# Performance work log

Measured on AMD Instinct MI355X. Metric: run time of the kernel, lower is better.

The kernel has to match this reference:

```python
import jax, jax.numpy as jnp
import numpy as np


def _gcn_conv(h, src, dst, W, b, n):
    # PyG GCNConv: x @ W, then symmetric-normalized aggregation with self-loops
    deg = jax.ops.segment_sum(jnp.ones(src.shape[0], h.dtype), dst, num_segments=n)
    dinv = jax.lax.rsqrt(jnp.maximum(deg, 1.0))  # deg >= 1 because self-loops are included
    norm = dinv[src] * dinv[dst]                 # [E]
    m = (h @ W)[src] * norm[:, None]             # gather + scale
    return jax.ops.segment_sum(m, dst, num_segments=n) + b


def setup_inputs() -> dict:
    key = jax.random.key(0)
    N, E, F, H, L, V = 50000, 800000, 128, 256, 64, 128
    ks = jax.random.split(key, 16)
    s = lambda fan_in: 1.0 / np.sqrt(fan_in)
    return {
        "x": jax.random.randint(ks[0], (N,), 0, V),
        "edge_index": jax.random.randint(ks[1], (2, E), 0, N),
        "eps": jax.random.normal(ks[2], (N, L), jnp.float32),
        "emb": jax.random.normal(ks[3], (V, F), jnp.float32),
        "W1": jax.random.normal(ks[4], (F, H), jnp.float32) * s(F),
        "b1": jnp.zeros((H,), jnp.float32),
        "W2": jax.random.normal(ks[5], (H, H), jnp.float32) * s(H),
        "b2": jnp.zeros((H,), jnp.float32),
        "Wmu": jax.random.normal(ks[6], (H, L), jnp.float32) * s(H),
        "bmu": jnp.zeros((L,), jnp.float32),
        "Wlv": jax.random.normal(ks[7], (H, L), jnp.float32) * s(H),
        "blv": jnp.zeros((L,), jnp.float32),
        "W3": jax.random.normal(ks[8], (L, H), jnp.float32) * s(L),
        "b3": jnp.zeros((H,), jnp.float32),
        "W4": jax.random.normal(ks[9], (H, V), jnp.float32) * s(H),
        "b4": jnp.zeros((V,), jnp.float32),
        "Wcap": jax.random.normal(ks[10], (L, 1), jnp.float32) * s(L),
        "bcap": jnp.zeros((1,), jnp.float32),
    }


def reference(x, edge_index, eps, emb, W1, b1, W2, b2, Wmu, bmu, Wlv, blv, W3, b3, W4, b4, Wcap, bcap):
    n = x.shape[0]
    loops = jnp.arange(n, dtype=edge_index.dtype)
    src = jnp.concatenate([edge_index[0], loops])  # add self-loops once, reuse
    dst = jnp.concatenate([edge_index[1], loops])

    h = emb[x]                                      # [N, F] embedding lookup
    h = jax.nn.relu(_gcn_conv(h, src, dst, W1, b1, n))
    h = jax.nn.relu(_gcn_conv(h, src, dst, W2, b2, n))
    mu = h @ Wmu + bmu
    logvar = h @ Wlv + blv
    z = mu + eps * jnp.exp(0.5 * logvar)            # reparameterize
    recon_x = jax.nn.relu(z @ W3 + b3) @ W4 + b4    # decode
    capitalize = jax.nn.sigmoid(z @ Wcap + bcap)
    return recon_x, capitalize, mu, logvar
```

## Files before the change

### kernel.cpp

```cpp
#include <hip/hip_runtime.h>
#include <math.h>


typedef __attribute__((ext_vector_type(8))) short bf16x8;
typedef __attribute__((ext_vector_type(4))) float f32x4;

__device__ inline unsigned short f2bf(float x) {
    unsigned u = __float_as_uint(x);
    return (unsigned short)((u + 0x7FFFu + ((u >> 16) & 1u)) >> 16);
}
__device__ inline float bf2f(unsigned short h) {
    return __uint_as_float(((unsigned)h) << 16);
}

__global__ __launch_bounds__(256) void k_deg_count(const int* __restrict__ dst,
                                                   int* __restrict__ degint, int E) {
    int e = blockIdx.x * 256 + threadIdx.x;
    if (e < E) atomicAdd(&degint[dst[e]], 1);
}

#define SCAN_BLOCK 1024
__global__ __launch_bounds__(SCAN_BLOCK) void k_scan_local(
        const int* __restrict__ degint, int* __restrict__ row_ptr,
        int* __restrict__ bsum, float* __restrict__ dinv, int N) {
    __shared__ int s[SCAN_BLOCK];
    int gid = blockIdx.x * SCAN_BLOCK + threadIdx.x;
    int d = (gid < N) ? (degint[gid] + 1) : 0;
    if (gid < N) dinv[gid] = rsqrtf((float)d);
    s[threadIdx.x] = d;
    __syncthreads();
    for (int off = 1; off < SCAN_BLOCK; off <<= 1) {
        int t = (threadIdx.x >= off) ? s[threadIdx.x - off] : 0;
        __syncthreads();
        s[threadIdx.x] += t;
        __syncthreads();
    }
    if (gid < N) row_ptr[gid] = s[threadIdx.x] - d;
    if (threadIdx.x == SCAN_BLOCK - 1) bsum[blockIdx.x] = s[SCAN_BLOCK - 1];
}

__global__ void k_scan_bsum(int* __restrict__ bsum, int nb) {
    if (blockIdx.x == 0 && threadIdx.x == 0) {
        int acc = 0;
        for (int i = 0; i < nb; ++i) { int v = bsum[i]; bsum[i] = acc; acc += v; }
    }
}

__global__ __launch_bounds__(256) void k_scan_add(int* __restrict__ row_ptr,
                                                  const int* __restrict__ bsum,
                                                  int N, int T) {
    int gid = blockIdx.x * 256 + threadIdx.x;
    if (gid < N) row_ptr[gid] += bsum[gid / SCAN_BLOCK];
    if (gid == 0) row_ptr[N] = T;
}

__global__ __launch_bounds__(256) void k_fill(
        const int* __restrict__ src, const int* __restrict__ dst,
        const int* __restrict__ x, const float* __restrict__ dinv,
        const int* __restrict__ row_ptr, int* __restrict__ cursor,
        int4* __restrict__ pack, int E, int N) {
    const int base = (blockIdx.x * 256 + threadIdx.x) * 4;
#pragma unroll
    for (int j = 0; j < 4; ++j) {
        int e = base + j;
        if (e < E) {
            int s = src[e], d = dst[e];
            float w = dinv[s] * dinv[d];
            int pos = row_ptr[d] + atomicAdd(&cursor[d], 1);
            pack[pos] = make_int4(__float_as_int(w), x[s], s, 0);
        } else if (e < E + N) {
            int i = e - E;
            float di = dinv[i];
            int pos = row_ptr[i] + atomicAdd(&cursor[i], 1);
            pack[pos] = make_int4(__float_as_int(di * di), x[i], i, 0);
        }
    }
}

__global__ __launch_bounds__(256) void k_cvt_all(
        const float* __restrict__ B0, unsigned short* __restrict__ h0, int K0, int N0,
        const float* __restrict__ B1, unsigned short* __restrict__ h1, int K1, int N1,
        const float* __restrict__ B2, unsigned short* __restrict__ h2, int K2, int N2,
        const float* __restrict__ B3, unsigned short* __restrict__ h3, int K3, int N3,
        const float* __restrict__ B4, unsigned short* __restrict__ h4, int K4, int N4) {
    const float* B; unsigned short* Bh; int K, Ncol;
    switch (blockIdx.y) {
        case 0: B = B0; Bh = h0; K = K0; Ncol = N0; break;
        case 1: B = B1; Bh = h1; K = K1; Ncol = N1; break;
        case 2: B = B2; Bh = h2; K = K2; Ncol = N2; break;
        case 3: B = B3; Bh = h3; K = K3; Ncol = N3; break;
        default: B = B4; Bh = h4; K = K4; Ncol = N4; break;
    }
    int i = blockIdx.x * 256 + threadIdx.x;
    if (i >= K * Ncol) return;
    int k = i / Ncol, n = i - k * Ncol;
    Bh[(long)n * K + k] = f2bf(B[i]);
}

__global__ __launch_bounds__(256) void k_gemm_f32t(
        const float* __restrict__ A, const float* __restrict__ B,
        unsigned short* __restrict__ CbT, int M, int K, int Ncol) {
    constexpr int BM = 64, BN = 64, BK = 16;
    __shared__ float As[BK][BM];
    __shared__ float Bs[BK][BN];
    const int tid = threadIdx.x;
    const int tx = tid & 15, ty = tid >> 4;
    const int rowBase = blockIdx.x * BM;
    const int colBase = blockIdx.y * BN;
    const int lr = tid >> 2, lc4 = tid & 3;
    const int br = tid >> 4, bc4 = tid & 15;
    const int arow = rowBase + lr;
    const int K4 = K >> 2, N4 = Ncol >> 2;
    const float4* A4 = (const float4*)A;
    const float4* B4 = (const float4*)B;
    float acc[4][4] = {{0.f}};
    for (int k0 = 0; k0 < K; k0 += BK) {
        float4 av = make_float4(0.f, 0.f, 0.f, 0.f);
        if (arow < M) av = A4[(long)arow * K4 + (k0 >> 2) + lc4];
        As[lc4 * 4 + 0][lr] = av.x;
        As[lc4 * 4 + 1][lr] = av.y;
        As[lc4 * 4 + 2][lr] = av.z;
        As[lc4 * 4 + 3][lr] = av.w;
        float4 bv = B4[(long)(k0 + br) * N4 + (colBase >> 2) + bc4];
        *(float4*)&Bs[br][bc4 * 4] = bv;
        __syncthreads();
#pragma unroll
        for (int k = 0; k < BK; ++k) {
            float4 a4v = *(const float4*)&As[k][ty * 4];
            float4 b4v = *(const float4*)&Bs[k][tx * 4];
            float aa[4] = {a4v.x, a4v.y, a4v.z, a4v.w};
            float bb[4] = {b4v.x, b4v.y, b4v.z, b4v.w};
#pragma unroll
            for (int i = 0; i < 4; ++i)
#pragma unroll
                for (int j = 0; j < 4; ++j)
                    acc[i][j] = fmaf(aa[i], bb[j], acc[i][j]);
        }
        __syncthreads();
    }
#pragma unroll
    for (int i = 0; i < 4; ++i) {
        int row = rowBase + ty * 4 + i;
        if (row < M) {
#pragma unroll
            for (int c = 0; c < 4; ++c) {
                int col = colBase + tx * 4 + c;
                CbT[(long)col * M + row] = f2bf(acc[i][c]);
            }
        }
    }
}

__global__ __launch_bounds__(256) void k_coef(
        const int4* __restrict__ pack, const int* __restrict__ row_ptr,
        unsigned short* __restrict__ cb, int N) {
    const int wave = threadIdx.x >> 6;
    const int lane = threadIdx.x & 63;
    const int node = blockIdx.x * 4 + wave;
    if (node >= N) return;
    const int tok0 = lane, tok1 = lane + 64;
    float c0 = 0.f, c1 = 0.f;
    const int beg = row_ptr[node], end = row_ptr[node + 1];
    int e = beg;
    for (; e + 4 <= end; e += 4) {
        int2 p0 = *(const int2*)&pack[e];
        int2 p1 = *(const int2*)&pack[e + 1];
        int2 p2 = *(const int2*)&pack[e + 2];
        int2 p3 = *(const int2*)&pack[e + 3];
        c0 += (p0.y == tok0) ? __int_as_float(p0.x) : 0.f;
        c1 += (p0.y == tok1) ? __int_as_float(p0.x) : 0.f;
        c0 += (p1.y == tok0) ? __int_as_float(p1.x) : 0.f;
        c1 += (p1.y == tok1) ? __int_as_float(p1.x) : 0.f;
        c0 += (p2.y == tok0) ? __int_as_float(p2.x) : 0.f;
        c1 += (p2.y == tok1) ? __int_as_float(p2.x) : 0.f;
        c0 += (p3.y == tok0) ? __int_as_float(p3.x) : 0.f;
        c1 += (p3.y == tok1) ? __int_as_float(p3.x) : 0.f;
    }
    for (; e < end; ++e) {
        int2 p = *(const int2*)&pack[e];
        c0 += (p.y == tok0) ? __int_as_float(p.x) : 0.f;
        c1 += (p.y == tok1) ? __int_as_float(p.x) : 0.f;
    }
    const long base = (long)node * 128;
    cb[base + lane]      = f2bf(c0);
    cb[base + lane + 64] = f2bf(c1);
}

template<bool RELU, bool BIAS, bool OUTBF>
__global__ __launch_bounds__(256) void k_gemm_mfma(
        const unsigned short* __restrict__ A, const unsigned short* __restrict__ Bt,
        const float* __restrict__ bias, float* __restrict__ Cf,
        unsigned short* __restrict__ Cb, int M, int K, int Ncol) {
    __shared__ unsigned short Ash[128][40];
    __shared__ unsigned short Bsh[64][40];
    const int tid = threadIdx.x;
    const int lane = tid & 63, w = tid >> 6;
    const int fr = lane & 15, quad = lane >> 4;
    const int wm0 = w * 32;
    const int rowBase = blockIdx.x * 128;
    const int colBase = blockIdx.y * 64;

    const int arow = tid >> 1;
    const int ahalf = (tid & 1) << 4;
    int agrow = rowBase + arow; if (agrow >= M) agrow = M - 1;
    const long abase = (long)agrow * K + ahalf;
    const int brow = tid >> 2;
    const int bseg = (tid & 3) << 3;
    const long bbase = (long)(colBase + brow) * K + bseg;

    f32x4 acc[2][4];
#pragma unroll
    for (int i = 0; i < 2; ++i)
#pragma unroll
        for (int j = 0; j < 4; ++j) acc[i][j] = (f32x4){0.f, 0.f, 0.f, 0.f};

    for (int k0 = 0; k0 < K; k0 += 32) {
        *(bf16x8*)&Ash[arow][ahalf]     = *(const bf16x8*)&A[abase + k0];
        *(bf16x8*)&Ash[arow][ahalf + 8] = *(const bf16x8*)&A[abase + k0 + 8];
        *(bf16x8*)&Bsh[brow][bseg]      = *(const bf16x8*)&Bt[bbase + k0];
        __syncthreads();
        bf16x8 ahf[2], bhf[4];
#pragma unroll
        for (int i = 0; i < 2; ++i)
            ahf[i] = *(const bf16x8*)&Ash[wm0 + i * 16 + fr][quad * 8];
#pragma unroll
        for (int j = 0; j < 4; ++j)
            bhf[j] = *(const bf16x8*)&Bsh[j * 16 + fr][quad * 8];
#pragma unroll
        for (int i = 0; i < 2; ++i)
#pragma unroll
            for (int j = 0; j < 4; ++j)
                acc[i][j] = __builtin_amdgcn_mfma_f32_16x16x32_bf16(
                    ahf[i], bhf[j], acc[i][j], 0, 0, 0);
        __syncthreads();
    }

#pragma unroll
    for (int i = 0; i < 2; ++i) {
        const int rowb = rowBase + wm0 + i * 16 + quad * 4;
#pragma unroll
        for (int j = 0; j < 4; ++j) {
            const int col = colBase + j * 16 + fr;
            const float bv = BIAS ? bias[col] : 0.f;
#pragma unroll
            for (int r = 0; r < 4; ++r) {
                const int row = rowb + r;
                if (row < M) {
                    float v = acc[i][j][r] + bv;
                    if (RELU) v = fmaxf(v, 0.f);
                    const long o = (long)row * Ncol + col;
                    if (OUTBF) Cb[o] = f2bf(v);
                    else       Cf[o] = v;
                }
            }
        }
    }
}

__global__ __launch_bounds__(256) void k_gemm_heads(
        const unsigned short* __restrict__ A, const unsigned short* __restrict__ Bt,
        const float* __restrict__ bmu, const float* __restrict__ blv,
        const float* __restrict__ eps, const float* __restrict__ Wcap,
        const float* __restrict__ bcap, float* __restrict__ mu,
        float* __restrict__ lv, unsigned short* __restrict__ Zh,
        float* __restrict__ cap, int M) {
    constexpr int K = 256;
    __shared__ unsigned short Ash[64][40];
    __shared__ unsigned short Bsh[128][40];
    const int tid = threadIdx.x;
    const int lane = tid & 63, w = tid >> 6;
    const int fr = lane & 15, quad = lane >> 4;
    const int wm0 = w * 16;
    const int rowBase = blockIdx.x * 64;

    const int arow = tid >> 2;
    const int aseg = (tid & 3) << 3;
    int agrow = rowBase + arow; if (agrow >= M) agrow = M - 1;
    const long abase = (long)agrow * K + aseg;
    const int brow = tid >> 1;
    const int bseg = (tid & 1) << 4;
    const long bbase = (long)brow * K + bseg;

    f32x4 acc[8];
#pragma unroll
    for (int j = 0; j < 8; ++j) acc[j] = (f32x4){0.f, 0.f, 0.f, 0.f};

    for (int k0 = 0; k0 < K; k0 += 32) {
        *(bf16x8*)&Ash[arow][aseg] = *(const bf16x8*)&A[abase + k0];
        *(bf16x8*)&Bsh[brow][bseg]     = *(const bf16x8*)&Bt[bbase + k0];
        *(bf16x8*)&Bsh[brow][bseg + 8] = *(const bf16x8*)&Bt[bbase + k0 + 8];
        __syncthreads();
        bf16x8 ahf = *(const bf16x8*)&Ash[wm0 + fr][quad * 8];
#pragma unroll
        for (int j = 0; j < 8; ++j) {
            bf16x8 bhf = *(const bf16x8*)&Bsh[j * 16 + fr][quad * 8];
            acc[j] = __builtin_amdgcn_mfma_f32_16x16x32_bf16(ahf, bhf, acc[j], 0, 0, 0);
        }
        __syncthreads();
    }

    float capacc[4] = {0.f, 0.f, 0.f, 0.f};
#pragma unroll
    for (int j = 0; j < 4; ++j) {
        const int c = j * 16 + fr;
        const float bm = bmu[c], bl = blv[c];
        const float wc = Wcap[c];
#pragma unroll
        for (int r = 0; r < 4; ++r) {
            const int row = rowBase + wm0 + quad * 4 + r;
            if (row < M) {
                const long o = (long)row * 64 + c;
                float mv = acc[j][r] + bm;
                float lvv = acc[j + 4][r] + bl;
                mu[o] = mv;
                lv[o] = lvv;
                float zz = fmaf(eps[o], expf(0.5f * lvv), mv);
                Zh[o] = f2bf(zz);
                capacc[r] = fmaf(zz, wc, capacc[r]);
            }
        }
    }
    const float b0 = bcap[0];
#pragma unroll
    for (int r = 0; r < 4; ++r) {
        float v = capacc[r];
        v += __shfl_xor(v, 1, 64);
        v += __shfl_xor(v, 2, 64);
        v += __shfl_xor(v, 4, 64);
        v += __shfl_xor(v, 8, 64);
        if (fr == 0) {
            const int row = rowBase + wm0 + quad * 4 + r;
            if (row < M) cap[row] = 1.f / (1.f + expf(-(v + b0)));
        }
    }
}

__global__ __launch_bounds__(256) void k_gemm_decode(
        const unsigned short* __restrict__ Zh, const unsigned short* __restrict__ W3t,
        const unsigned short* __restrict__ W4t, const float* __restrict__ b3,
        const float* __restrict__ b4, float* __restrict__ recon, int M) {
    __shared__ unsigned short Zs[64][40];
    __shared__ unsigned short Bsh[256][40];
    __shared__ unsigned short Ts[64][264];
    const int tid = threadIdx.x;
    const int lane = tid & 63, w = tid >> 6;
    const int fr = lane & 15, quad = lane >> 4;
    const int wm0 = w * 16;
    const int rowBase = blockIdx.x * 64;

    const int zrow = tid & 63;
    const int zseg = (tid >> 6) << 3;
    int zgrow = rowBase + zrow; if (zgrow >= M) zgrow = M - 1;
    const long zbase = (long)zgrow * 64 + zseg;

    f32x4 acc1[16];
#pragma unroll
    for (int j = 0; j < 16; ++j) acc1[j] = (f32x4){0.f, 0.f, 0.f, 0.f};

#pragma unroll
    for (int k0 = 0; k0 < 64; k0 += 32) {
        *(bf16x8*)&Zs[zrow][zseg] = *(const bf16x8*)&Zh[zbase + k0 - zseg + zseg];
        __syncthreads();
        __syncthreads();
        break;
    }
#pragma unroll
    for (int j = 0; j < 16; ++j) acc1[j] = (f32x4){0.f, 0.f, 0.f, 0.f};
    for (int k0 = 0; k0 < 64; k0 += 32) {
        *(bf16x8*)&Zs[zrow][zseg] = *(const bf16x8*)&Zh[(long)zgrow * 64 + k0 + zseg];
        {
            const long wb = (long)tid * 64 + k0;
            *(bf16x8*)&Bsh[tid][0]  = *(const bf16x8*)&W3t[wb];
            *(bf16x8*)&Bsh[tid][8]  = *(const bf16x8*)&W3t[wb + 8];
            *(bf16x8*)&Bsh[tid][16] = *(const bf16x8*)&W3t[wb + 16];
            *(bf16x8*)&Bsh[tid][24] = *(const bf16x8*)&W3t[wb + 24];
        }
        __syncthreads();
        bf16x8 af = *(const bf16x8*)&Zs[wm0 + fr][quad * 8];
#pragma unroll
        for (int j = 0; j < 16; ++j) {
            bf16x8 bf = *(const bf16x8*)&Bsh[j * 16 + fr][quad * 8];
            acc1[j] = __builtin_amdgcn_mfma_f32_16x16x32_bf16(af, bf, acc1[j], 0, 0, 0);
        }
        __syncthreads();
    }

#pragma unroll
    for (int j = 0; j < 16; ++j) {
        const int col = j * 16 + fr;
        const float bv = b3[col];
#pragma unroll
        for (int r = 0; r < 4; ++r) {
            const int rl = wm0 + quad * 4 + r;
            Ts[rl][col] = f2bf(fmaxf(acc1[j][r] + bv, 0.f));
        }
    }
    __syncthreads();

    f32x4 acc2[8];
#pragma unroll
    for (int j = 0; j < 8; ++j) acc2[j] = (f32x4){0.f, 0.f, 0.f, 0.f};
    const int br2 = tid >> 1;
    const int bs2 = (tid & 1) << 4;
    for (int k0 = 0; k0 < 256; k0 += 32) {
        const long wb = (long)br2 * 256 + k0 + bs2;
        *(bf16x8*)&Bsh[br2][bs2]     = *(const bf16x8*)&W4t[wb];
        *(bf16x8*)&Bsh[br2][bs2 + 8] = *(const bf16x8*)&W4t[wb + 8];
        __syncthreads();
        bf16x8 at = *(const bf16x8*)&Ts[wm0 + fr][k0 + quad * 8];
#pragma unroll
        for (int j = 0; j < 8; ++j) {
            bf16x8 bf = *(const bf16x8*)&Bsh[j * 16 + fr][quad * 8];
            acc2[j] = __builtin_amdgcn_mfma_f32_16x16x32_bf16(at, bf, acc2[j], 0, 0, 0);
        }
        __syncthreads();
    }

#pragma unroll
    for (int j = 0; j < 8; ++j) {
        const int col = j * 16 + fr;
        const float bv = b4[col];
#pragma unroll
        for (int r = 0; r < 4; ++r) {
            const int row = rowBase + wm0 + quad * 4 + r;
            if (row < M) recon[(long)row * 128 + col] = acc2[j][r] + bv;
        }
    }
}

__global__ __launch_bounds__(256) void k_agg_nb(
        const unsigned short* __restrict__ h1, const int* __restrict__ row_ptr,
        const int4* __restrict__ pack, unsigned short* __restrict__ Ob, int N) {
    const int wave = threadIdx.x >> 6;
    const int lane = threadIdx.x & 63;
    const int node = blockIdx.x * 4 + wave;
    if (node >= N) return;
    const ushort4* h4 = (const ushort4*)h1;
    float ax = 0.f, ay = 0.f, az = 0.f, aw = 0.f;
    const int beg = row_ptr[node], end = row_ptr[node + 1];
    int e = beg;
    for (; e + 8 <= end; e += 8) {
        int4 p0 = pack[e],     p1 = pack[e + 1], p2 = pack[e + 2], p3 = pack[e + 3];
        int4 p4 = pack[e + 4], p5 = pack[e + 5], p6 = pack[e + 6], p7 = pack[e + 7];
        ushort4 v0 = h4[(long)p0.z * 64 + lane];
        ushort4 v1 = h4[(long)p1.z * 64 + lane];
        ushort4 v2 = h4[(long)p2.z * 64 + lane];
        ushort4 v3 = h4[(long)p3.z * 64 + lane];
        ushort4 v4 = h4[(long)p4.z * 64 + lane];
        ushort4 v5 = h4[(long)p5.z * 64 + lane];
        ushort4 v6 = h4[(long)p6.z * 64 + lane];
        ushort4 v7 = h4[(long)p7.z * 64 + lane];
        float w0 = __int_as_float(p0.x), w1 = __int_as_float(p1.x);
        float w2 = __int_as_float(p2.x), w3 = __int_as_float(p3.x);
        float w4 = __int_as_float(p4.x), w5 = __int_as_float(p5.x);
        float w6 = __int_as_float(p6.x), w7 = __int_as_float(p7.x);
        ax = fmaf(bf2f(v0.x), w0, ax); ay = fmaf(bf2f(v0.y), w0, ay);
        az = fmaf(bf2f(v0.z), w0, az); aw = fmaf(bf2f(v0.w), w0, aw);
        ax = fmaf(bf2f(v1.x), w1, ax); ay = fmaf(bf2f(v1.y), w1, ay);
        az = fmaf(bf2f(v1.z), w1, az); aw = fmaf(bf2f(v1.w), w1, aw);
        ax = fmaf(bf2f(v2.x), w2, ax); ay = fmaf(bf2f(v2.y), w2, ay);
        az = fmaf(bf2f(v2.z), w2, az); aw = fmaf(bf2f(v2.w), w2, aw);
        ax = fmaf(bf2f(v3.x), w3, ax); ay = fmaf(bf2f(v3.y), w3, ay);
        az = fmaf(bf2f(v3.z), w3, az); aw = fmaf(bf2f(v3.w), w3, aw);
        ax = fmaf(bf2f(v4.x), w4, ax); ay = fmaf(bf2f(v4.y), w4, ay);
        az = fmaf(bf2f(v4.z), w4, az); aw = fmaf(bf2f(v4.w), w4, aw);
        ax = fmaf(bf2f(v5.x), w5, ax); ay = fmaf(bf2f(v5.y), w5, ay);
        az = fmaf(bf2f(v5.z), w5, az); aw = fmaf(bf2f(v5.w), w5, aw);
        ax = fmaf(bf2f(v6.x), w6, ax); ay = fmaf(bf2f(v6.y), w6, ay);
        az = fmaf(bf2f(v6.z), w6, az); aw = fmaf(bf2f(v6.w), w6, aw);
        ax = fmaf(bf2f(v7.x), w7, ax); ay = fmaf(bf2f(v7.y), w7, ay);
        az = fmaf(bf2f(v7.z), w7, az); aw = fmaf(bf2f(v7.w), w7, aw);
    }
    for (; e + 4 <= end; e += 4) {
        int4 p0 = pack[e], p1 = pack[e + 1], p2 = pack[e + 2], p3 = pack[e + 3];
        ushort4 v0 = h4[(long)p0.z * 64 + lane];
        ushort4 v1 = h4[(long)p1.z * 64 + lane];
        ushort4 v2 = h4[(long)p2.z * 64 + lane];
        ushort4 v3 = h4[(long)p3.z * 64 + lane];
        float w0 = __int_as_float(p0.x), w1 = __int_as_float(p1.x);
        float w2 = __int_as_float(p2.x), w3 = __int_as_float(p3.x);
        ax = fmaf(bf2f(v0.x), w0, ax); ay = fmaf(bf2f(v0.y), w0, ay);
        az = fmaf(bf2f(v0.z), w0, az); aw = fmaf(bf2f(v0.w), w0, aw);
        ax = fmaf(bf2f(v1.x), w1, ax); ay = fmaf(bf2f(v1.y), w1, ay);
        az = fmaf(bf2f(v1.z), w1, az); aw = fmaf(bf2f(v1.w), w1, aw);
        ax = fmaf(bf2f(v2.x), w2, ax); ay = fmaf(bf2f(v2.y), w2, ay);
        az = fmaf(bf2f(v2.z), w2, az); aw = fmaf(bf2f(v2.w), w2, aw);
        ax = fmaf(bf2f(v3.x), w3, ax); ay = fmaf(bf2f(v3.y), w3, ay);
        az = fmaf(bf2f(v3.z), w3, az); aw = fmaf(bf2f(v3.w), w3, aw);
    }
    for (; e < end; ++e) {
        int4 p = pack[e];
        float w0 = __int_as_float(p.x);
        ushort4 v = h4[(long)p.z * 64 + lane];
        ax = fmaf(bf2f(v.x), w0, ax); ay = fmaf(bf2f(v.y), w0, ay);
        az = fmaf(bf2f(v.z), w0, az); aw = fmaf(bf2f(v.w), w0, aw);
    }
    ushort4 o;
    o.x = f2bf(ax); o.y = f2bf(ay); o.z = f2bf(az); o.w = f2bf(aw);
    ((ushort4*)Ob)[(long)node * 64 + lane] = o;
}

extern "C" void kernel_launch(void* const* d_in, const int* in_sizes, int n_in,
                              void* d_out, int out_size, void* d_ws, size_t ws_size,
                              hipStream_t stream) {
    const int*   x    = (const int*)d_in[0];
    const int*   ei   = (const int*)d_in[1];
    const float* eps  = (const float*)d_in[2];
    const float* emb  = (const float*)d_in[3];
    const float* W1   = (const float*)d_in[4];
    const float* b1   = (const float*)d_in[5];
    const float* W2   = (const float*)d_in[6];
    const float* b2   = (const float*)d_in[7];
    const float* Wmu  = (const float*)d_in[8];
    const float* bmu  = (const float*)d_in[9];
    const float* Wlv  = (const float*)d_in[10];
    const float* blv  = (const float*)d_in[11];
    const float* W3   = (const float*)d_in[12];
    const float* b3   = (const float*)d_in[13];
    const float* W4   = (const float*)d_in[14];
    const float* b4   = (const float*)d_in[15];
    const float* Wcap = (const float*)d_in[16];
    const float* bcap = (const float*)d_in[17];

    const int N = in_sizes[0];
    const int E = in_sizes[1] / 2;
    const int H = in_sizes[5];
    const int L = in_sizes[9];
    const int V = in_sizes[15];
    const int F = in_sizes[4] / H;
    const int T = E + N;

    const int* src = ei;
    const int* dst = ei + E;

    char* w = (char*)d_ws;
    unsigned short* h1b  = (unsigned short*)w; w += (size_t)N * H * 2;
    unsigned short* a2b  = (unsigned short*)w; w += (size_t)N * H * 2;
    unsigned short* h2b  = (unsigned short*)w; w += (size_t)N * H * 2;
    unsigned short* zh   = (unsigned short*)w; w += (size_t)N * L * 2;
    unsigned short* cb   = (unsigned short*)w; w += (size_t)N * V * 2;
    int*   degint = (int*)w;   w += (size_t)N * 4;
    int*   cursor = (int*)w;   w += (size_t)N * 4;
    int*   rowp   = (int*)w;   w += (size_t)(N + 1) * 4;
    float* dinv   = (float*)w; w += (size_t)N * 4;
    int*   bsum   = (int*)w;   w += 256 * 4;
    int4*  pack   = (int4*)w;  w += (size_t)T * 16;
    unsigned short* tabT = (unsigned short*)w; w += (size_t)H * V * 2;
    unsigned short* W2t  = (unsigned short*)w; w += (size_t)H * H * 2;
    unsigned short* Wml  = (unsigned short*)w; w += (size_t)H * 2 * L * 2;
    unsigned short* W3t  = (unsigned short*)w; w += (size_t)L * H * 2;
    unsigned short* W4t  = (unsigned short*)w; w += (size_t)H * V * 2;

    float* outp    = (float*)d_out;
    float* recon   = outp;
    float* cap     = outp + (size_t)N * V;
    float* mu      = outp + (size_t)N * V + N;
    float* logvar  = mu + (size_t)N * L;

    const int nN  = (N + 255) / 256;
    const int nE  = (E + 255) / 256;
    const int nT4 = (T + 1023) / 1024;
    const int nSc = (N + SCAN_BLOCK - 1) / SCAN_BLOCK;
    const int gM128 = (N + 127) / 128;
    const int gM64  = (N + 63) / 64;

    hipMemsetAsync(degint, 0, (size_t)N * 8, stream);
    k_deg_count<<<nE, 256, 0, stream>>>(dst, degint, E);
    k_scan_local<<<nSc, SCAN_BLOCK, 0, stream>>>(degint, rowp, bsum, dinv, N);
    k_scan_bsum<<<1, 64, 0, stream>>>(bsum, nSc);
    k_scan_add<<<nN, 256, 0, stream>>>(rowp, bsum, N, T);
    k_fill<<<nT4, 256, 0, stream>>>(src, dst, x, dinv, rowp, cursor, pack, E, N);

    k_cvt_all<<<dim3((H * H + 255) / 256, 5), 256, 0, stream>>>(
        W2, W2t, H, H,
        Wmu, Wml, H, L,
        Wlv, Wml + (size_t)L * H, H, L,
        W3, W3t, L, H,
        W4, W4t, H, V);

    k_gemm_f32t<<<dim3(V / 64, H / 64), 256, 0, stream>>>(emb, W1, tabT, V, F, H);
    k_coef<<<(N + 3) / 4, 256, 0, stream>>>(pack, rowp, cb, N);
    k_gemm_mfma<true, true, true><<<dim3(gM128, H / 64), 256, 0, stream>>>(
        cb, tabT, b1, nullptr, h1b, N, V, H);

    k_agg_nb<<<(N + 3) / 4, 256, 0, stream>>>(h1b, rowp, pack, a2b, N);
    k_gemm_mfma<true, true, true><<<dim3(gM128, H / 64), 256, 0, stream>>>(
        a2b, W2t, b2, nullptr, h2b, N, H, H);

    k_gemm_heads<<<gM64, 256, 0, stream>>>(
        h2b, Wml, bmu, blv, eps, Wcap, bcap, mu, logvar, zh, cap, N);

    k_gemm_decode<<<gM64, 256, 0, stream>>>(zh, W3t, W4t, b3, b4, recon, N);
}
```

Measured before the change: 409.4 us.

## Use full-width 256-column GEMM tiles and half-wave 16-byte gathers in aggregation

Replaces the 128x64-tile GEMM with a 64x256 tile, so each block computes all 256 output columns and the A tile is read once instead of four times across column blocks. The pack layout is reordered so the weight and source index sit in the first 8 bytes. The aggregation kernel now reads only those 8 bytes as int2 and splits each wave into two halves that gather different edges with 16-byte row loads, then combines the halves with a shuffle. The coef kernel now loads full int4 records to reach the token field, and a dead loop is removed from the decoder. The larger B tile in shared memory and the 16 accumulators per lane raise register and LDS pressure, which may lower occupancy.

```diff
diff --git a/kernel.cpp b/kernel.cpp
--- a/kernel.cpp
+++ b/kernel.cpp
@@ -3,6 +3,7 @@
 
 
 typedef __attribute__((ext_vector_type(8))) short bf16x8;
+typedef __attribute__((ext_vector_type(8))) unsigned short u16x8;
 typedef __attribute__((ext_vector_type(4))) float f32x4;
 
 __device__ inline unsigned short f2bf(float x) {
@@ -67,12 +68,12 @@
             int s = src[e], d = dst[e];
             float w = dinv[s] * dinv[d];
             int pos = row_ptr[d] + atomicAdd(&cursor[d], 1);
-            pack[pos] = make_int4(__float_as_int(w), x[s], s, 0);
+            pack[pos] = make_int4(__float_as_int(w), s, x[s], 0);
         } else if (e < E + N) {
             int i = e - E;
             float di = dinv[i];
             int pos = row_ptr[i] + atomicAdd(&cursor[i], 1);
-            pack[pos] = make_int4(__float_as_int(di * di), x[i], i, 0);
+            pack[pos] = make_int4(__float_as_int(di * di), i, x[i], 0);
         }
     }
 }
@@ -163,95 +164,81 @@
     const int beg = row_ptr[node], end = row_ptr[node + 1];
     int e = beg;
     for (; e + 4 <= end; e += 4) {
-        int2 p0 = *(const int2*)&pack[e];
-        int2 p1 = *(const int2*)&pack[e + 1];
-        int2 p2 = *(const int2*)&pack[e + 2];
-        int2 p3 = *(const int2*)&pack[e + 3];
-        c0 += (p0.y == tok0) ? __int_as_float(p0.x) : 0.f;
-        c1 += (p0.y == tok1) ? __int_as_float(p0.x) : 0.f;
-        c0 += (p1.y == tok0) ? __int_as_float(p1.x) : 0.f;
-        c1 += (p1.y == tok1) ? __int_as_float(p1.x) : 0.f;
-        c0 += (p2.y == tok0) ? __int_as_float(p2.x) : 0.f;
-        c1 += (p2.y == tok1) ? __int_as_float(p2.x) : 0.f;
-        c0 += (p3.y == tok0) ? __int_as_float(p3.x) : 0.f;
-        c1 += (p3.y == tok1) ? __int_as_float(p3.x) : 0.f;
+        int4 p0 = pack[e];
+        int4 p1 = pack[e + 1];
+        int4 p2 = pack[e + 2];
+        int4 p3 = pack[e + 3];
+        c0 += (p0.z == tok0) ? __int_as_float(p0.x) : 0.f;
+        c1 += (p0.z == tok1) ? __int_as_float(p0.x) : 0.f;
+        c0 += (p1.z == tok0) ? __int_as_float(p1.x) : 0.f;
+        c1 += (p1.z == tok1) ? __int_as_float(p1.x) : 0.f;
+        c0 += (p2.z == tok0) ? __int_as_float(p2.x) : 0.f;
+        c1 += (p2.z == tok1) ? __int_as_float(p2.x) : 0.f;
+        c0 += (p3.z == tok0) ? __int_as_float(p3.x) : 0.f;
+        c1 += (p3.z == tok1) ? __int_as_float(p3.x) : 0.f;
     }
     for (; e < end; ++e) {
-        int2 p = *(const int2*)&pack[e];
-        c0 += (p.y == tok0) ? __int_as_float(p.x) : 0.f;
-        c1 += (p.y == tok1) ? __int_as_float(p.x) : 0.f;
+        int4 p = pack[e];
+        c0 += (p.z == tok0) ? __int_as_float(p.x) : 0.f;
+        c1 += (p.z == tok1) ? __int_as_float(p.x) : 0.f;
     }
     const long base = (long)node * 128;
     cb[base + lane]      = f2bf(c0);
     cb[base + lane + 64] = f2bf(c1);
 }
 
-template<bool RELU, bool BIAS, bool OUTBF>
-__global__ __launch_bounds__(256) void k_gemm_mfma(
+template<bool RELU>
+__global__ __launch_bounds__(256) void k_gemm_bn256(
         const unsigned short* __restrict__ A, const unsigned short* __restrict__ Bt,
-        const float* __restrict__ bias, float* __restrict__ Cf,
-        unsigned short* __restrict__ Cb, int M, int K, int Ncol) {
-    __shared__ unsigned short Ash[128][40];
-    __shared__ unsigned short Bsh[64][40];
+        const float* __restrict__ bias, unsigned short* __restrict__ Cb,
+        int M, int K) {
+    __shared__ unsigned short Ash[64][40];
+    __shared__ unsigned short Bsh[256][40];
     const int tid = threadIdx.x;
     const int lane = tid & 63, w = tid >> 6;
     const int fr = lane & 15, quad = lane >> 4;
-    const int wm0 = w * 32;
-    const int rowBase = blockIdx.x * 128;
-    const int colBase = blockIdx.y * 64;
-
-    const int arow = tid >> 1;
-    const int ahalf = (tid & 1) << 4;
+    const int wm0 = w * 16;
+    const int rowBase = blockIdx.x * 64;
+
+    const int arow = tid & 63;
+    const int aseg = (tid >> 6) << 3;
     int agrow = rowBase + arow; if (agrow >= M) agrow = M - 1;
-    const long abase = (long)agrow * K + ahalf;
-    const int brow = tid >> 2;
-    const int bseg = (tid & 3) << 3;
-    const long bbase = (long)(colBase + brow) * K + bseg;
-
-    f32x4 acc[2][4];
-#pragma unroll
-    for (int i = 0; i < 2; ++i)
-#pragma unroll
-        for (int j = 0; j < 4; ++j) acc[i][j] = (f32x4){0.f, 0.f, 0.f, 0.f};
+    const long abase = (long)agrow * K + aseg;
+
+    f32x4 acc[16];
+#pragma unroll
+    for (int j = 0; j < 16; ++j) acc[j] = (f32x4){0.f, 0.f, 0.f, 0.f};
 
     for (int k0 = 0; k0 < K; k0 += 32) {
-        *(bf16x8*)&Ash[arow][ahalf]     = *(const bf16x8*)&A[abase + k0];
-        *(bf16x8*)&Ash[arow][ahalf + 8] = *(const bf16x8*)&A[abase + k0 + 8];
-        *(bf16x8*)&Bsh[brow][bseg]      = *(const bf16x8*)&Bt[bbase + k0];
-        __syncthreads();
-        bf16x8 ahf[2], bhf[4];
-#pragma unroll
-        for (int i = 0; i < 2; ++i)
-            ahf[i] = *(const bf16x8*)&Ash[wm0 + i * 16 + fr][quad * 8];
-#pragma unroll
-        for (int j = 0; j < 4; ++j)
-            bhf[j] = *(const bf16x8*)&Bsh[j * 16 + fr][quad * 8];
-#pragma unroll
-        for (int i = 0; i < 2; ++i)
-#pragma unroll
-            for (int j = 0; j < 4; ++j)
-                acc[i][j] = __builtin_amdgcn_mfma_f32_16x16x32_bf16(
-                    ahf[i], bhf[j], acc[i][j], 0, 0, 0);
-        __syncthreads();
-    }
-
-#pragma unroll
-    for (int i = 0; i < 2; ++i) {
-        const int rowb = rowBase + wm0 + i * 16 + quad * 4;
-#pragma unroll
-        for (int j = 0; j < 4; ++j) {
-            const int col = colBase + j * 16 + fr;
-            const float bv = BIAS ? bias[col] : 0.f;
-#pragma unroll
-            for (int r = 0; r < 4; ++r) {
-                const int row = rowb + r;
-                if (row < M) {
-                    float v = acc[i][j][r] + bv;
-                    if (RELU) v = fmaxf(v, 0.f);
-                    const long o = (long)row * Ncol + col;
-                    if (OUTBF) Cb[o] = f2bf(v);
-                    else       Cf[o] = v;
-                }
+        *(bf16x8*)&Ash[arow][aseg] = *(const bf16x8*)&A[abase + k0];
+        {
+            const long wb = (long)tid * K + k0;
+            *(bf16x8*)&Bsh[tid][0]  = *(const bf16x8*)&Bt[wb];
+            *(bf16x8*)&Bsh[tid][8]  = *(const bf16x8*)&Bt[wb + 8];
+            *(bf16x8*)&Bsh[tid][16] = *(const bf16x8*)&Bt[wb + 16];
+            *(bf16x8*)&Bsh[tid][24] = *(const bf16x8*)&Bt[wb + 24];
+        }
+        __syncthreads();
+        bf16x8 af = *(const bf16x8*)&Ash[wm0 + fr][quad * 8];
+#pragma unroll
+        for (int j = 0; j < 16; ++j) {
+            bf16x8 bfv = *(const bf16x8*)&Bsh[j * 16 + fr][quad * 8];
+            acc[j] = __builtin_amdgcn_mfma_f32_16x16x32_bf16(af, bfv, acc[j], 0, 0, 0);
+        }
+        __syncthreads();
+    }
+
+#pragma unroll
+    for (int j = 0; j < 16; ++j) {
+        const int col = j * 16 + fr;
+        const float bv = bias[col];
+#pragma unroll
+        for (int r = 0; r < 4; ++r) {
+            const int row = rowBase + wm0 + quad * 4 + r;
+            if (row < M) {
+                float v = acc[j][r] + bv;
+                if (RELU) v = fmaxf(v, 0.f);
+                Cb[(long)row * 256 + col] = f2bf(v);
             }
         }
     }
@@ -351,19 +338,8 @@
     const int zrow = tid & 63;
     const int zseg = (tid >> 6) << 3;
     int zgrow = rowBase + zrow; if (zgrow >= M) zgrow = M - 1;
-    const long zbase = (long)zgrow * 64 + zseg;
 
     f32x4 acc1[16];
-#pragma unroll
-    for (int j = 0; j < 16; ++j) acc1[j] = (f32x4){0.f, 0.f, 0.f, 0.f};
-
-#pragma unroll
-    for (int k0 = 0; k0 < 64; k0 += 32) {
-        *(bf16x8*)&Zs[zrow][zseg] = *(const bf16x8*)&Zh[zbase + k0 - zseg + zseg];
-        __syncthreads();
-        __syncthreads();
-        break;
-    }
 #pragma unroll
     for (int j = 0; j < 16; ++j) acc1[j] = (f32x4){0.f, 0.f, 0.f, 0.f};
     for (int k0 = 0; k0 < 64; k0 += 32) {
@@ -430,74 +406,58 @@
 
 __global__ __launch_bounds__(256) void k_agg_nb(
         const unsigned short* __restrict__ h1, const int* __restrict__ row_ptr,
-        const int4* __restrict__ pack, unsigned short* __restrict__ Ob, int N) {
+        const int2* __restrict__ pk2, unsigned short* __restrict__ Ob, int N) {
     const int wave = threadIdx.x >> 6;
     const int lane = threadIdx.x & 63;
     const int node = blockIdx.x * 4 + wave;
     if (node >= N) return;
-    const ushort4* h4 = (const ushort4*)h1;
-    float ax = 0.f, ay = 0.f, az = 0.f, aw = 0.f;
+    const int half = lane >> 5;
+    const int col  = lane & 31;
+    const u16x8* hrow = (const u16x8*)h1;
+    float acc[8] = {0.f, 0.f, 0.f, 0.f, 0.f, 0.f, 0.f, 0.f};
     const int beg = row_ptr[node], end = row_ptr[node + 1];
     int e = beg;
     for (; e + 8 <= end; e += 8) {
-        int4 p0 = pack[e],     p1 = pack[e + 1], p2 = pack[e + 2], p3 = pack[e + 3];
-        int4 p4 = pack[e + 4], p5 = pack[e + 5], p6 = pack[e + 6], p7 = pack[e + 7];
-        ushort4 v0 = h4[(long)p0.z * 64 + lane];
-        ushort4 v1 = h4[(long)p1.z * 64 + lane];
-        ushort4 v2 = h4[(long)p2.z * 64 + lane];
-        ushort4 v3 = h4[(long)p3.z * 64 + lane];
-        ushort4 v4 = h4[(long)p4.z * 64 + lane];
-        ushort4 v5 = h4[(long)p5.z * 64 + lane];
-        ushort4 v6 = h4[(long)p6.z * 64 + lane];
-        ushort4 v7 = h4[(long)p7.z * 64 + lane];
-        float w0 = __int_as_float(p0.x), w1 = __int_as_float(p1.x);
-        float w2 = __int_as_float(p2.x), w3 = __int_as_float(p3.x);
-        float w4 = __int_as_float(p4.x), w5 = __int_as_float(p5.x);
-        float w6 = __int_as_float(p6.x), w7 = __int_as_float(p7.x);
-        ax = fmaf(bf2f(v0.x), w0, ax); ay = fmaf(bf2f(v0.y), w0, ay);
-        az = fmaf(bf2f(v0.z), w0, az); aw = fmaf(bf2f(v0.w), w0, aw);
-        ax = fmaf(bf2f(v1.x), w1, ax); ay = fmaf(bf2f(v1.y), w1, ay);
-        az = fmaf(bf2f(v1.z), w1, az); aw = fmaf(bf2f(v1.w), w1, aw);
-        ax = fmaf(bf2f(v2.x), w2, ax); ay = fmaf(bf2f(v2.y), w2, ay);
-        az = fmaf(bf2f(v2.z), w2, az); aw = fmaf(bf2f(v2.w), w2, aw);
-        ax = fmaf(bf2f(v3.x), w3, ax); ay = fmaf(bf2f(v3.y), w3, ay);
-        az = fmaf(bf2f(v3.z), w3, az); aw = fmaf(bf2f(v3.w), w3, aw);
-        ax = fmaf(bf2f(v4.x), w4, ax); ay = fmaf(bf2f(v4.y), w4, ay);
-        az = fmaf(bf2f(v4.z), w4, az); aw = fmaf(bf2f(v4.w), w4, aw);
-        ax = fmaf(bf2f(v5.x), w5, ax); ay = fmaf(bf2f(v5.y), w5, ay);
-        az = fmaf(bf2f(v5.z), w5, az); aw = fmaf(bf2f(v5.w), w5, aw);
-        ax = fmaf(bf2f(v6.x), w6, ax); ay = fmaf(bf2f(v6.y), w6, ay);
-        az = fmaf(bf2f(v6.z), w6, az); aw = fmaf(bf2f(v6.w), w6, aw);
-        ax = fmaf(bf2f(v7.x), w7, ax); ay = fmaf(bf2f(v7.y), w7, ay);
-        az = fmaf(bf2f(v7.z), w7, az); aw = fmaf(bf2f(v7.w), w7, aw);
-    }
-    for (; e + 4 <= end; e += 4) {
-        int4 p0 = pack[e], p1 = pack[e + 1], p2 = pack[e + 2], p3 = pack[e + 3];
-        ushort4 v0 = h4[(long)p0.z * 64 + lane];
-        ushort4 v1 = h4[(long)p1.z * 64 + lane];
-        ushort4 v2 = h4[(long)p2.z * 64 + lane];
-        ushort4 v3 = h4[(long)p3.z * 64 + lane];
-        float w0 = __int_as_float(p0.x), w1 = __int_as_float(p1.x);
-        float w2 = __int_as_float(p2.x), w3 = __int_as_float(p3.x);
-        ax = fmaf(bf2f(v0.x), w0, ax); ay = fmaf(bf2f(v0.y), w0, ay);
-        az = fmaf(bf2f(v0.z), w0, az); aw = fmaf(bf2f(v0.w), w0, aw);
-        ax = fmaf(bf2f(v1.x), w1, ax); ay = fmaf(bf2f(v1.y), w1, ay);
-        az = fmaf(bf2f(v1.z), w1, az); aw = fmaf(bf2f(v1.w), w1, aw);
-        ax = fmaf(bf2f(v2.x), w2, ax); ay = fmaf(bf2f(v2.y), w2, ay);
-        az = fmaf(bf2f(v2.z), w2, az); aw = fmaf(bf2f(v2.w), w2, aw);
-        ax = fmaf(bf2f(v3.x), w3, ax); ay = fmaf(bf2f(v3.y), w3, ay);
-        az = fmaf(bf2f(v3.z), w3, az); aw = fmaf(bf2f(v3.w), w3, aw);
-    }
-    for (; e < end; ++e) {
-        int4 p = pack[e];
-        float w0 = __int_as_float(p.x);
-        ushort4 v = h4[(long)p.z * 64 + lane];
-        ax = fmaf(bf2f(v.x), w0, ax); ay = fmaf(bf2f(v.y), w0, ay);
-        az = fmaf(bf2f(v.z), w0, az); aw = fmaf(bf2f(v.w), w0, aw);
-    }
-    ushort4 o;
-    o.x = f2bf(ax); o.y = f2bf(ay); o.z = f2bf(az); o.w = f2bf(aw);
-    ((ushort4*)Ob)[(long)node * 64 + lane] = o;
+        int2 q0 = pk2[2 * (e + 0 + half)];
+        int2 q1 = pk2[2 * (e + 2 + half)];
+        int2 q2 = pk2[2 * (e + 4 + half)];
+        int2 q3 = pk2[2 * (e + 6 + half)];
+        u16x8 v0 = hrow[(long)q0.y * 32 + col];
+        u16x8 v1 = hrow[(long)q1.y * 32 + col];
+        u16x8 v2 = hrow[(long)q2.y * 32 + col];
+        u16x8 v3 = hrow[(long)q3.y * 32 + col];
+        float w0 = __int_as_float(q0.x), w1 = __int_as_float(q1.x);
+        float w2 = __int_as_float(q2.x), w3 = __int_as_float(q3.x);
+#pragma unroll
+        for (int c = 0; c < 8; ++c) {
+            acc[c] = fmaf(bf2f(v0[c]), w0, acc[c]);
+            acc[c] = fmaf(bf2f(v1[c]), w1, acc[c]);
+            acc[c] = fmaf(bf2f(v2[c]), w2, acc[c]);
+            acc[c] = fmaf(bf2f(v3[c]), w3, acc[c]);
+        }
+    }
+    for (; e + 2 <= end; e += 2) {
+        int2 q = pk2[2 * (e + half)];
+        float w = __int_as_float(q.x);
+        u16x8 v = hrow[(long)q.y * 32 + col];
+#pragma unroll
+        for (int c = 0; c < 8; ++c) acc[c] = fmaf(bf2f(v[c]), w, acc[c]);
+    }
+    if (e < end) {
+        int2 q = pk2[2 * e];
+        float w = (half == 0) ? __int_as_float(q.x) : 0.f;
+        u16x8 v = hrow[(long)q.y * 32 + col];
+#pragma unroll
+        for (int c = 0; c < 8; ++c) acc[c] = fmaf(bf2f(v[c]), w, acc[c]);
+    }
+#pragma unroll
+    for (int c = 0; c < 8; ++c) acc[c] += __shfl_xor(acc[c], 32, 64);
+    if (lane < 32) {
+        u16x8 o;
+#pragma unroll
+        for (int c = 0; c < 8; ++c) o[c] = f2bf(acc[c]);
+        ((u16x8*)Ob)[(long)node * 32 + col] = o;
+    }
 }
 
 extern "C" void kernel_launch(void* const* d_in, const int* in_sizes, int n_in,
@@ -561,7 +521,6 @@
     const int nE  = (E + 255) / 256;
     const int nT4 = (T + 1023) / 1024;
     const int nSc = (N + SCAN_BLOCK - 1) / SCAN_BLOCK;
-    const int gM128 = (N + 127) / 128;
     const int gM64  = (N + 63) / 64;
 
     hipMemsetAsync(degint, 0, (size_t)N * 8, stream);
@@ -580,12 +539,10 @@
 
     k_gemm_f32t<<<dim3(V / 64, H / 64), 256, 0, stream>>>(emb, W1, tabT, V, F, H);
     k_coef<<<(N + 3) / 4, 256, 0, stream>>>(pack, rowp, cb, N);
-    k_gemm_mfma<true, true, true><<<dim3(gM128, H / 64), 256, 0, stream>>>(
-        cb, tabT, b1, nullptr, h1b, N, V, H);
-
-    k_agg_nb<<<(N + 3) / 4, 256, 0, stream>>>(h1b, rowp, pack, a2b, N);
-    k_gemm_mfma<true, true, true><<<dim3(gM128, H / 64), 256, 0, stream>>>(
-        a2b, W2t, b2, nullptr, h2b, N, H, H);
+    k_gemm_bn256<true><<<gM64, 256, 0, stream>>>(cb, tabT, b1, h1b, N, V);
+
+    k_agg_nb<<<(N + 3) / 4, 256, 0, stream>>>(h1b, rowp, (const int2*)pack, a2b, N);
+    k_gemm_bn256<true><<<gM64, 256, 0, stream>>>(a2b, W2t, b2, h2b, N, H);
 
     k_gemm_heads<<<gM64, 256, 0, stream>>>(
         h2b, Wml, bmu, blv, eps, Wcap, bcap, mu, logvar, zh, cap, N);
```

Measured after the change: 429.2 us. 1.05x slower.
